# Optimization experiments

Hardware: AMD Instinct MI355X
Metric: run time of the kernel (lower is better)

## Reference

```python
import jax, jax.numpy as jnp
import numpy as np

HID = 128          # hidden_dim
NF = 8             # n_features of reconstructed PathFeatureExtractor
S0 = 100.0
T = 1.0
XI0 = 0.235 ** 2
ETA_REF = 1.9
DELTA_IDX = 3      # PathFeatureExtractor.DELTA_PREV_INDEX
NEG_SLOPE = 0.2


def _features(S):
    """Causal per-step path features. S: (B, n+1) -> (B, n, NF)."""
    B, np1 = S.shape
    n = np1 - 1
    logm = jnp.log(S / S0)                       # (B, n+1) log-moneyness
    x = logm[:, :n]                              # value at step k
    ret = jnp.diff(logm, axis=1)                 # (B, n) log returns
    qv_full = jnp.cumsum(ret ** 2, axis=1)
    qv = jnp.concatenate([jnp.zeros((B, 1), S.dtype), qv_full[:, :-1]], axis=1)  # QV up to step k
    k = jnp.arange(n, dtype=S.dtype)
    t = k / n * T
    tau = (T - t) / T                            # normalized time to maturity
    run_mean = jnp.cumsum(x, axis=1) / (k + 1.0)
    ones = jnp.ones_like(x)
    feats = jnp.stack([
        x,                                       # 0: log(S_k/S0)
        tau * ones,                              # 1: time to maturity
        jnp.sqrt(XI0) * ones,                    # 2: ref vol
        jnp.zeros_like(x),                       # 3: delta_prev slot (injected in scan)
        run_mean,                                # 4: running mean log-price (sig level 1)
        qv,                                      # 5: realized quadratic variation (sig level 2 diag)
        ETA_REF * jnp.sqrt(qv + 1e-12),          # 6: vol-of-vol scaled QV
        (t / T) * ones,                          # 7: elapsed time
    ], axis=-1)
    return feats


def _mlp(feat, W0, b0, rW1, rb1, rW2, rb2, sW1, sb1, sW2, sb2, Wf, bf):
    lrelu = lambda v: jax.nn.leaky_relu(v, NEG_SLOPE)
    h = lrelu(feat @ W0 + b0)
    h = h + (lrelu(h @ rW1 + rb1) @ rW2 + rb2)   # ResidualBlock 1
    h = h + (lrelu(h @ sW1 + sb1) @ sW2 + sb2)   # ResidualBlock 2
    return jax.nn.sigmoid(h @ Wf + bf)[:, 0]


def _linear_params(key, fan_in, fan_out):
    kw, kb = jax.random.split(key)
    bound = 1.0 / np.sqrt(fan_in)
    W = jax.random.uniform(kw, (fan_in, fan_out), jnp.float32, -bound, bound)
    b = jax.random.uniform(kb, (fan_out,), jnp.float32, -bound, bound)
    return W, b


def setup_inputs() -> dict:
    key = jax.random.key(0)
    ks = jax.random.split(key, 6)
    B, n = 32768, 64
    # GBM-like price paths starting at S0
    incr = 0.02 * jax.random.normal(ks[0], (B, n), jnp.float32)
    logpath = jnp.concatenate([jnp.zeros((B, 1), jnp.float32), jnp.cumsum(incr, axis=1)], axis=1)
    S = S0 * jnp.exp(logpath)
    W0, b0 = _linear_params(ks[1], NF, HID)
    rW1, rb1 = _linear_params(ks[2], HID, HID)
    rW2, rb2 = _linear_params(jax.random.fold_in(ks[2], 1), HID, HID)
    sW1, sb1 = _linear_params(ks[3], HID, HID)
    sW2, sb2 = _linear_params(jax.random.fold_in(ks[3], 1), HID, HID)
    Wf, bf = _linear_params(ks[4], HID, 1)
    return {"S": S, "W0": W0, "b0": b0, "rW1": rW1, "rb1": rb1, "rW2": rW2, "rb2": rb2,
            "sW1": sW1, "sb1": sb1, "sW2": sW2, "sb2": sb2, "Wf": Wf, "bf": bf}


def reference(S, W0, b0, rW1, rb1, rW2, rb2, sW1, sb1, sW2, sb2, Wf, bf):
    feats = _features(S).astype(jnp.float32)          # (B, n, NF)
    fT = jnp.transpose(feats, (1, 0, 2))              # (n, B, NF) for scan
    B = S.shape[0]

    def step(delta_prev, feat_k):
        # inject detached delta_{k-1} at feature index 3 (matches .detach())
        feat_k = feat_k.at[:, DELTA_IDX].set(jax.lax.stop_gradient(delta_prev))
        d = _mlp(feat_k, W0, b0, rW1, rb1, rW2, rb2, sW1, sb1, sW2, sb2, Wf, bf)
        return d, d

    _, deltas = jax.lax.scan(step, jnp.zeros((B,), jnp.float32), fT)
    return jnp.transpose(deltas)                      # (B, n)
```

## Files before the change

kernel.cpp:

```cpp
#include <hip/hip_runtime.h>
#include <math.h>

#define HID 128
#define NSTEPS 64
#define SLEN 65
#define THREADS 256
#define ROWS 64
#define ASTRIDE 136
#define FSTRIDE 40
#define DSTR 68

typedef _Float16 half8 __attribute__((ext_vector_type(8)));
typedef __fp16 fp16x2 __attribute__((ext_vector_type(2)));
typedef float floatx4 __attribute__((ext_vector_type(4)));

__global__ __launch_bounds__(THREADS, 2)
void hedger(const float* __restrict__ S,
            const float* __restrict__ W0,  const float* __restrict__ b0,
            const float* __restrict__ rW1, const float* __restrict__ rb1,
            const float* __restrict__ rW2, const float* __restrict__ rb2,
            const float* __restrict__ sW1, const float* __restrict__ sb1,
            const float* __restrict__ sW2, const float* __restrict__ sb2,
            const float* __restrict__ Wf,  const float* __restrict__ bfp,
            float* __restrict__ out)
{
  __shared__ __align__(16) _Float16 bufA[ROWS * ASTRIDE];
  __shared__ __align__(16) _Float16 bufB[ROWS * ASTRIDE];
  __shared__ __align__(16) _Float16 featb[ROWS * FSTRIDE];
  __shared__ __align__(16) _Float16 WfS[HID];
  __shared__ __align__(16) _Float16 Ws2S[HID];
  __shared__             float    CvalS;
  __shared__ __align__(16) float    Slds[ROWS * SLEN];
  __shared__ __align__(16) float    deltab[ROWS * DSTR];

  const int tid  = threadIdx.x;
  const int wave = tid >> 6;
  const int lane = tid & 63;
  const int l15  = lane & 15;
  const int quad = lane >> 4;
  const int n_base = wave * 32;
  const int r0 = blockIdx.x * ROWS;
  const int col0 = n_base + 2 * l15;

  half8 wfrag[3][4][2];
  {
    const float* Wm[3] = {rW1, rW2, sW1};
#pragma unroll
    for (int m = 0; m < 3; ++m)
#pragma unroll
      for (int kq = 0; kq < 4; ++kq)
#pragma unroll
        for (int nt = 0; nt < 2; ++nt) {
          const int n  = col0 + nt;
          const int kb = kq * 32 + quad * 8;
          half8 f;
#pragma unroll
          for (int j = 0; j < 8; ++j)
            f[j] = (_Float16)Wm[m][(kb + j) * HID + n];
          wfrag[m][kq][nt] = f;
        }
  }
  half8 w0frag[2];
#pragma unroll
  for (int nt = 0; nt < 2; ++nt) {
    const int n = col0 + nt;
    half8 f;
#pragma unroll
    for (int j = 0; j < 8; ++j) {
      const int k = quad * 8 + j;
      f[j] = (k < 8) ? (_Float16)W0[k * HID + n] : (_Float16)0.f;
    }
    w0frag[nt] = f;
  }
  float b0r[2], rb1r[2], rb2r[2], sb1r[2];
#pragma unroll
  for (int nt = 0; nt < 2; ++nt) {
    const int n = col0 + nt;
    b0r[nt] = b0[n]; rb1r[nt] = rb1[n]; rb2r[nt] = rb2[n]; sb1r[nt] = sb1[n];
  }

  for (int i = tid; i < ROWS * FSTRIDE; i += THREADS) featb[i] = (_Float16)0.f;
  if (tid < HID) {
    WfS[tid] = (_Float16)Wf[tid];
    float s = 0.f;
    for (int n = 0; n < HID; ++n) s += sW2[tid * HID + n] * Wf[n];
    Ws2S[tid] = (_Float16)s;
  }
  if (wave == 0) {
    float p = sb2[lane] * Wf[lane] + sb2[lane + 64] * Wf[lane + 64];
    p += __shfl_xor(p, 1);  p += __shfl_xor(p, 2);  p += __shfl_xor(p, 4);
    p += __shfl_xor(p, 8);  p += __shfl_xor(p, 16); p += __shfl_xor(p, 32);
    if (lane == 0) CvalS = p + bfp[0];
  }
  for (int i = tid; i < ROWS * SLEN; i += THREADS)
    Slds[i] = S[(size_t)r0 * SLEN + i];
  __syncthreads();
  const float Cval = CvalS;

  float lm_prev = 0.f, cum_x = 0.f, qv = 0.f;
  const float* Srow = &Slds[(tid & (ROWS - 1)) * SLEN];
  if (tid < ROWS) {
    const float lm = logf(Srow[0] * 0.01f);
    lm_prev = lm; cum_x = lm; qv = 0.f;
    _Float16* fr = &featb[tid * FSTRIDE];
    fr[0] = (_Float16)lm;
    fr[1] = (_Float16)1.0f;
    fr[2] = (_Float16)0.235f;
    fr[3] = (_Float16)0.f;
    fr[4] = (_Float16)lm;
    fr[5] = (_Float16)0.f;
    fr[6] = (_Float16)(1.9f * sqrtf(1e-12f));
    fr[7] = (_Float16)0.f;
  }
  __syncthreads();

  floatx4 acc[4][2];

#define INIT_BIAS(BR) do { \
  _Pragma("unroll") for (int mt = 0; mt < 4; ++mt) \
  _Pragma("unroll") for (int nt = 0; nt < 2; ++nt) { \
    floatx4 z = {BR[nt], BR[nt], BR[nt], BR[nt]}; acc[mt][nt] = z; } } while (0)

#define INIT_BIAS_RES(BR, RESBUF) do { \
  _Pragma("unroll") for (int mt = 0; mt < 4; ++mt) \
  _Pragma("unroll") for (int r = 0; r < 4; ++r) { \
    const int row = mt * 16 + quad * 4 + r; \
    const fp16x2 h2 = *(const fp16x2*)&RESBUF[row * ASTRIDE + col0]; \
    acc[mt][0][r] = BR[0] + (float)h2[0]; \
    acc[mt][1][r] = BR[1] + (float)h2[1]; \
  } } while (0)

#define GEMM128(SRC, MI) do { \
  _Pragma("unroll") for (int kq = 0; kq < 4; ++kq) { \
    half8 afr[4]; \
    _Pragma("unroll") for (int mt = 0; mt < 4; ++mt) \
      afr[mt] = *(const half8*)&SRC[(mt * 16 + l15) * ASTRIDE + kq * 32 + quad * 8]; \
    _Pragma("unroll") for (int mt = 0; mt < 4; ++mt) \
    _Pragma("unroll") for (int nt = 0; nt < 2; ++nt) \
      acc[mt][nt] = __builtin_amdgcn_mfma_f32_16x16x32_f16( \
          afr[mt], wfrag[MI][kq][nt], acc[mt][nt], 0, 0, 0); \
  } } while (0)

#define EPI_LRELU(DST) do { \
  _Pragma("unroll") for (int mt = 0; mt < 4; ++mt) \
  _Pragma("unroll") for (int r = 0; r < 4; ++r) { \
    const int row = mt * 16 + quad * 4 + r; \
    const float v0 = acc[mt][0][r]; \
    const float v1 = acc[mt][1][r]; \
    fp16x2 h2 = {(__fp16)fmaxf(v0, 0.2f * v0), (__fp16)fmaxf(v1, 0.2f * v1)}; \
    *(fp16x2*)&DST[row * ASTRIDE + col0] = h2; \
  } } while (0)

#define EPI_STORE(DST) do { \
  _Pragma("unroll") for (int mt = 0; mt < 4; ++mt) \
  _Pragma("unroll") for (int r = 0; r < 4; ++r) { \
    const int row = mt * 16 + quad * 4 + r; \
    fp16x2 h2 = {(__fp16)acc[mt][0][r], (__fp16)acc[mt][1][r]}; \
    *(fp16x2*)&DST[row * ASTRIDE + col0] = h2; \
  } } while (0)

#pragma unroll 1
  for (int k = 0; k < NSTEPS; ++k) {
    INIT_BIAS(b0r);
    {
      half8 afr[4];
#pragma unroll
      for (int mt = 0; mt < 4; ++mt)
        afr[mt] = *(const half8*)&featb[(mt * 16 + l15) * FSTRIDE + quad * 8];
#pragma unroll
      for (int mt = 0; mt < 4; ++mt)
#pragma unroll
        for (int nt = 0; nt < 2; ++nt)
          acc[mt][nt] = __builtin_amdgcn_mfma_f32_16x16x32_f16(
              afr[mt], w0frag[nt], acc[mt][nt], 0, 0, 0);
    }
    EPI_LRELU(bufA);
    __syncthreads();

    if (tid < ROWS) {
      const int kk = k + 1;
      const float lm = logf(Srow[kk] * 0.01f);
      const float rr = lm - lm_prev; qv += rr * rr;
      lm_prev = lm; cum_x += lm;
      const float tT = (float)kk * (1.f / 64.f);
      _Float16* fr = &featb[tid * FSTRIDE];
      fr[0] = (_Float16)lm;
      fr[1] = (_Float16)(1.f - tT);
      fr[4] = (_Float16)(cum_x / (float)(kk + 1));
      fr[5] = (_Float16)qv;
      fr[6] = (_Float16)(1.9f * sqrtf(qv + 1e-12f));
      fr[7] = (_Float16)tT;
    }

    INIT_BIAS(rb1r);            GEMM128(bufA, 0); EPI_LRELU(bufB);
    __syncthreads();
    INIT_BIAS_RES(rb2r, bufA);  GEMM128(bufB, 1); EPI_STORE(bufA);
    __syncthreads();
    INIT_BIAS(sb1r);            GEMM128(bufA, 2); EPI_LRELU(bufB);
    __syncthreads();

    {
      floatx4 dacc  = {0.f, 0.f, 0.f, 0.f};
      floatx4 dacc2 = {0.f, 0.f, 0.f, 0.f};
#pragma unroll
      for (int kq = 0; kq < 4; ++kq) {
        const int off = kq * 32 + quad * 8;
        const half8 a1 = *(const half8*)&bufA[(wave * 16 + l15) * ASTRIDE + off];
        const half8 w1 = *(const half8*)&WfS[off];
        dacc  = __builtin_amdgcn_mfma_f32_16x16x32_f16(a1, w1, dacc, 0, 0, 0);
        const half8 a2 = *(const half8*)&bufB[(wave * 16 + l15) * ASTRIDE + off];
        const half8 w2 = *(const half8*)&Ws2S[off];
        dacc2 = __builtin_amdgcn_mfma_f32_16x16x32_f16(a2, w2, dacc2, 0, 0, 0);
      }
      if (l15 < 4) {
        const float s1 = (l15 & 2) ? ((l15 & 1) ? dacc[3] : dacc[2])
                                   : ((l15 & 1) ? dacc[1] : dacc[0]);
        const float s2 = (l15 & 2) ? ((l15 & 1) ? dacc2[3] : dacc2[2])
                                   : ((l15 & 1) ? dacc2[1] : dacc2[0]);
        const int row = wave * 16 + quad * 4 + l15;
        const float d = 1.f / (1.f + expf(-(s1 + s2 + Cval)));
        featb[row * FSTRIDE + 3] = (_Float16)d;
        deltab[row * DSTR + k] = d;
      }
    }
    __syncthreads();
  }

  {
    const int row = tid >> 2;
    const int c0  = (tid & 3) * 16;
    const float* dr = &deltab[row * DSTR + c0];
    float* orow = &out[(size_t)(r0 + row) * NSTEPS + c0];
#pragma unroll
    for (int u = 0; u < 4; ++u) {
      const floatx4 v = *(const floatx4*)&dr[u * 4];
      *(floatx4*)&orow[u * 4] = v;
    }
  }
#undef INIT_BIAS
#undef INIT_BIAS_RES
#undef GEMM128
#undef EPI_LRELU
#undef EPI_STORE
}

extern "C" void kernel_launch(void* const* d_in, const int* in_sizes, int n_in,
                              void* d_out, int out_size, void* d_ws, size_t ws_size,
                              hipStream_t stream) {
  const float* S   = (const float*)d_in[0];
  const float* W0  = (const float*)d_in[1];
  const float* b0  = (const float*)d_in[2];
  const float* rW1 = (const float*)d_in[3];
  const float* rb1 = (const float*)d_in[4];
  const float* rW2 = (const float*)d_in[5];
  const float* rb2 = (const float*)d_in[6];
  const float* sW1 = (const float*)d_in[7];
  const float* sb1 = (const float*)d_in[8];
  const float* sW2 = (const float*)d_in[9];
  const float* sb2 = (const float*)d_in[10];
  const float* Wf  = (const float*)d_in[11];
  const float* bf  = (const float*)d_in[12];
  float* out = (float*)d_out;

  const int B = out_size / NSTEPS;
  const int nblocks = B / ROWS;
  hedger<<<nblocks, THREADS, 0, stream>>>(
      S, W0, b0, rW1, rb1, rW2, rb2, sW1, sb1, sW2, sb2, Wf, bf, out);
}
```

Baseline: 345.6 us.

## Fold residual block's second linear into next layer weights to drop a barrier

Precomputes rW2·sW1 per block as a fused weight, so the second residual block's pre-activation becomes bufA·sW1 + bufB·(rW2·sW1) + (rb2·sW1 + sb1). The per-step stage that materialised h after block 1 is removed, along with one barrier per step. The final readout adds a third dot product using rW2·Wf, plus the matching bias constant. It also drops the S staging in LDS and reads S directly from global memory. The trade-off is more LDS (a third buffer), an extra fp16 rounding of the fused weights, and a per-block setup GEMM.

```diff
diff --git a/kernel.cpp b/kernel.cpp
--- a/kernel.cpp
+++ b/kernel.cpp
@@ -26,11 +26,12 @@
 {
   __shared__ __align__(16) _Float16 bufA[ROWS * ASTRIDE];
   __shared__ __align__(16) _Float16 bufB[ROWS * ASTRIDE];
+  __shared__ __align__(16) _Float16 bufC[ROWS * ASTRIDE];
   __shared__ __align__(16) _Float16 featb[ROWS * FSTRIDE];
   __shared__ __align__(16) _Float16 WfS[HID];
+  __shared__ __align__(16) _Float16 WfuS[HID];
   __shared__ __align__(16) _Float16 Ws2S[HID];
   __shared__             float    CvalS;
-  __shared__ __align__(16) float    Slds[ROWS * SLEN];
   __shared__ __align__(16) float    deltab[ROWS * DSTR];
 
   const int tid  = threadIdx.x;
@@ -44,9 +45,9 @@
 
   half8 wfrag[3][4][2];
   {
-    const float* Wm[3] = {rW1, rW2, sW1};
-#pragma unroll
-    for (int m = 0; m < 3; ++m)
+    const float* Wm[2] = {rW1, sW1};
+#pragma unroll
+    for (int m = 0; m < 2; ++m)
 #pragma unroll
       for (int kq = 0; kq < 4; ++kq)
 #pragma unroll
@@ -72,33 +73,113 @@
     }
     w0frag[nt] = f;
   }
-  float b0r[2], rb1r[2], rb2r[2], sb1r[2];
+  float b0r[2], rb1r[2], cv[2];
 #pragma unroll
   for (int nt = 0; nt < 2; ++nt) {
     const int n = col0 + nt;
-    b0r[nt] = b0[n]; rb1r[nt] = rb1[n]; rb2r[nt] = rb2[n]; sb1r[nt] = sb1[n];
+    b0r[nt] = b0[n]; rb1r[nt] = rb1[n];
+    float p = 0.f;
+#pragma unroll
+    for (int kq = 0; kq < 4; ++kq) {
+      const int kb = kq * 32 + quad * 8;
+#pragma unroll
+      for (int j = 0; j < 8; ++j)
+        p += rb2[kb + j] * (float)wfrag[1][kq][nt][j];
+    }
+    p += __shfl_xor(p, 16);
+    p += __shfl_xor(p, 32);
+    cv[nt] = p + sb1[n];
   }
 
   for (int i = tid; i < ROWS * FSTRIDE; i += THREADS) featb[i] = (_Float16)0.f;
   if (tid < HID) {
     WfS[tid] = (_Float16)Wf[tid];
-    float s = 0.f;
-    for (int n = 0; n < HID; ++n) s += sW2[tid * HID + n] * Wf[n];
-    Ws2S[tid] = (_Float16)s;
+    float su = 0.f, ss = 0.f;
+    for (int n = 0; n < HID; ++n) {
+      su += rW2[tid * HID + n] * Wf[n];
+      ss += sW2[tid * HID + n] * Wf[n];
+    }
+    WfuS[tid] = (_Float16)su;
+    Ws2S[tid] = (_Float16)ss;
   }
   if (wave == 0) {
-    float p = sb2[lane] * Wf[lane] + sb2[lane + 64] * Wf[lane + 64];
+    float p = (rb2[lane] + sb2[lane]) * Wf[lane]
+            + (rb2[lane + 64] + sb2[lane + 64]) * Wf[lane + 64];
     p += __shfl_xor(p, 1);  p += __shfl_xor(p, 2);  p += __shfl_xor(p, 4);
     p += __shfl_xor(p, 8);  p += __shfl_xor(p, 16); p += __shfl_xor(p, 32);
     if (lane == 0) CvalS = p + bfp[0];
   }
-  for (int i = tid; i < ROWS * SLEN; i += THREADS)
-    Slds[i] = S[(size_t)r0 * SLEN + i];
+
+  floatx4 acc[4][2];
+
+#define INIT_BIAS(BR) do { \
+  _Pragma("unroll") for (int mt = 0; mt < 4; ++mt) \
+  _Pragma("unroll") for (int nt = 0; nt < 2; ++nt) { \
+    floatx4 z = {BR[nt], BR[nt], BR[nt], BR[nt]}; acc[mt][nt] = z; } } while (0)
+
+#define GEMM128(SRC, MI) do { \
+  _Pragma("unroll") for (int kq = 0; kq < 4; ++kq) { \
+    half8 afr[4]; \
+    _Pragma("unroll") for (int mt = 0; mt < 4; ++mt) \
+      afr[mt] = *(const half8*)&SRC[(mt * 16 + l15) * ASTRIDE + kq * 32 + quad * 8]; \
+    _Pragma("unroll") for (int mt = 0; mt < 4; ++mt) \
+    _Pragma("unroll") for (int nt = 0; nt < 2; ++nt) \
+      acc[mt][nt] = __builtin_amdgcn_mfma_f32_16x16x32_f16( \
+          afr[mt], wfrag[MI][kq][nt], acc[mt][nt], 0, 0, 0); \
+  } } while (0)
+
+#define EPI_LRELU(DST) do { \
+  _Pragma("unroll") for (int mt = 0; mt < 4; ++mt) \
+  _Pragma("unroll") for (int r = 0; r < 4; ++r) { \
+    const int row = mt * 16 + quad * 4 + r; \
+    const float v0 = acc[mt][0][r]; \
+    const float v1 = acc[mt][1][r]; \
+    fp16x2 h2 = {(__fp16)fmaxf(v0, 0.2f * v0), (__fp16)fmaxf(v1, 0.2f * v1)}; \
+    *(fp16x2*)&DST[row * ASTRIDE + col0] = h2; \
+  } } while (0)
+
+#define EPI_STORE(DST) do { \
+  _Pragma("unroll") for (int mt = 0; mt < 4; ++mt) \
+  _Pragma("unroll") for (int r = 0; r < 4; ++r) { \
+    const int row = mt * 16 + quad * 4 + r; \
+    fp16x2 h2 = {(__fp16)acc[mt][0][r], (__fp16)acc[mt][1][r]}; \
+    *(fp16x2*)&DST[row * ASTRIDE + col0] = h2; \
+  } } while (0)
+
+#pragma unroll 1
+  for (int h = 0; h < 2; ++h) {
+    __syncthreads();
+    for (int i = tid; i < ROWS * HID; i += THREADS) {
+      const int row = i >> 7, c = i & 127;
+      bufA[row * ASTRIDE + c] = (_Float16)rW2[(h * 64 + row) * HID + c];
+    }
+    __syncthreads();
+    {
+      float zr[2] = {0.f, 0.f};
+      INIT_BIAS(zr);
+      GEMM128(bufA, 1);
+      EPI_STORE(bufB);
+    }
+    __syncthreads();
+#pragma unroll
+    for (int kqh = 0; kqh < 2; ++kqh) {
+      const int kq = h * 2 + kqh;
+      half8 f0, f1;
+#pragma unroll
+      for (int j = 0; j < 8; ++j) {
+        const int kl = kq * 32 + quad * 8 + j - h * 64;
+        const fp16x2 p = *(const fp16x2*)&bufB[kl * ASTRIDE + col0];
+        f0[j] = (_Float16)p[0];
+        f1[j] = (_Float16)p[1];
+      }
+      wfrag[2][kq][0] = f0;
+      wfrag[2][kq][1] = f1;
+    }
+  }
   __syncthreads();
-  const float Cval = CvalS;
 
   float lm_prev = 0.f, cum_x = 0.f, qv = 0.f;
-  const float* Srow = &Slds[(tid & (ROWS - 1)) * SLEN];
+  const float* Srow = S + (size_t)(r0 + (tid & (ROWS - 1))) * SLEN;
   if (tid < ROWS) {
     const float lm = logf(Srow[0] * 0.01f);
     lm_prev = lm; cum_x = lm; qv = 0.f;
@@ -113,51 +194,7 @@
     fr[7] = (_Float16)0.f;
   }
   __syncthreads();
-
-  floatx4 acc[4][2];
-
-#define INIT_BIAS(BR) do { \
-  _Pragma("unroll") for (int mt = 0; mt < 4; ++mt) \
-  _Pragma("unroll") for (int nt = 0; nt < 2; ++nt) { \
-    floatx4 z = {BR[nt], BR[nt], BR[nt], BR[nt]}; acc[mt][nt] = z; } } while (0)
-
-#define INIT_BIAS_RES(BR, RESBUF) do { \
-  _Pragma("unroll") for (int mt = 0; mt < 4; ++mt) \
-  _Pragma("unroll") for (int r = 0; r < 4; ++r) { \
-    const int row = mt * 16 + quad * 4 + r; \
-    const fp16x2 h2 = *(const fp16x2*)&RESBUF[row * ASTRIDE + col0]; \
-    acc[mt][0][r] = BR[0] + (float)h2[0]; \
-    acc[mt][1][r] = BR[1] + (float)h2[1]; \
-  } } while (0)
-
-#define GEMM128(SRC, MI) do { \
-  _Pragma("unroll") for (int kq = 0; kq < 4; ++kq) { \
-    half8 afr[4]; \
-    _Pragma("unroll") for (int mt = 0; mt < 4; ++mt) \
-      afr[mt] = *(const half8*)&SRC[(mt * 16 + l15) * ASTRIDE + kq * 32 + quad * 8]; \
-    _Pragma("unroll") for (int mt = 0; mt < 4; ++mt) \
-    _Pragma("unroll") for (int nt = 0; nt < 2; ++nt) \
-      acc[mt][nt] = __builtin_amdgcn_mfma_f32_16x16x32_f16( \
-          afr[mt], wfrag[MI][kq][nt], acc[mt][nt], 0, 0, 0); \
-  } } while (0)
-
-#define EPI_LRELU(DST) do { \
-  _Pragma("unroll") for (int mt = 0; mt < 4; ++mt) \
-  _Pragma("unroll") for (int r = 0; r < 4; ++r) { \
-    const int row = mt * 16 + quad * 4 + r; \
-    const float v0 = acc[mt][0][r]; \
-    const float v1 = acc[mt][1][r]; \
-    fp16x2 h2 = {(__fp16)fmaxf(v0, 0.2f * v0), (__fp16)fmaxf(v1, 0.2f * v1)}; \
-    *(fp16x2*)&DST[row * ASTRIDE + col0] = h2; \
-  } } while (0)
-
-#define EPI_STORE(DST) do { \
-  _Pragma("unroll") for (int mt = 0; mt < 4; ++mt) \
-  _Pragma("unroll") for (int r = 0; r < 4; ++r) { \
-    const int row = mt * 16 + quad * 4 + r; \
-    fp16x2 h2 = {(__fp16)acc[mt][0][r], (__fp16)acc[mt][1][r]}; \
-    *(fp16x2*)&DST[row * ASTRIDE + col0] = h2; \
-  } } while (0)
+  const float Cval = CvalS;
 
 #pragma unroll 1
   for (int k = 0; k < NSTEPS; ++k) {
@@ -192,33 +229,42 @@
       fr[7] = (_Float16)tT;
     }
 
-    INIT_BIAS(rb1r);            GEMM128(bufA, 0); EPI_LRELU(bufB);
-    __syncthreads();
-    INIT_BIAS_RES(rb2r, bufA);  GEMM128(bufB, 1); EPI_STORE(bufA);
-    __syncthreads();
-    INIT_BIAS(sb1r);            GEMM128(bufA, 2); EPI_LRELU(bufB);
+    INIT_BIAS(rb1r);  GEMM128(bufA, 0);  EPI_LRELU(bufB);
+    __syncthreads();
+
+    INIT_BIAS(cv);
+    GEMM128(bufA, 1);
+    GEMM128(bufB, 2);
+    EPI_LRELU(bufC);
     __syncthreads();
 
     {
-      floatx4 dacc  = {0.f, 0.f, 0.f, 0.f};
-      floatx4 dacc2 = {0.f, 0.f, 0.f, 0.f};
+      floatx4 d1 = {0.f, 0.f, 0.f, 0.f};
+      floatx4 d2 = {0.f, 0.f, 0.f, 0.f};
+      floatx4 d3 = {0.f, 0.f, 0.f, 0.f};
+      const int arow = (wave * 16 + l15) * ASTRIDE;
 #pragma unroll
       for (int kq = 0; kq < 4; ++kq) {
         const int off = kq * 32 + quad * 8;
-        const half8 a1 = *(const half8*)&bufA[(wave * 16 + l15) * ASTRIDE + off];
+        const half8 a1 = *(const half8*)&bufA[arow + off];
         const half8 w1 = *(const half8*)&WfS[off];
-        dacc  = __builtin_amdgcn_mfma_f32_16x16x32_f16(a1, w1, dacc, 0, 0, 0);
-        const half8 a2 = *(const half8*)&bufB[(wave * 16 + l15) * ASTRIDE + off];
-        const half8 w2 = *(const half8*)&Ws2S[off];
-        dacc2 = __builtin_amdgcn_mfma_f32_16x16x32_f16(a2, w2, dacc2, 0, 0, 0);
+        d1 = __builtin_amdgcn_mfma_f32_16x16x32_f16(a1, w1, d1, 0, 0, 0);
+        const half8 a2 = *(const half8*)&bufB[arow + off];
+        const half8 w2 = *(const half8*)&WfuS[off];
+        d2 = __builtin_amdgcn_mfma_f32_16x16x32_f16(a2, w2, d2, 0, 0, 0);
+        const half8 a3 = *(const half8*)&bufC[arow + off];
+        const half8 w3 = *(const half8*)&Ws2S[off];
+        d3 = __builtin_amdgcn_mfma_f32_16x16x32_f16(a3, w3, d3, 0, 0, 0);
       }
       if (l15 < 4) {
-        const float s1 = (l15 & 2) ? ((l15 & 1) ? dacc[3] : dacc[2])
-                                   : ((l15 & 1) ? dacc[1] : dacc[0]);
-        const float s2 = (l15 & 2) ? ((l15 & 1) ? dacc2[3] : dacc2[2])
-                                   : ((l15 & 1) ? dacc2[1] : dacc2[0]);
+        const float s1 = (l15 & 2) ? ((l15 & 1) ? d1[3] : d1[2])
+                                   : ((l15 & 1) ? d1[1] : d1[0]);
+        const float s2 = (l15 & 2) ? ((l15 & 1) ? d2[3] : d2[2])
+                                   : ((l15 & 1) ? d2[1] : d2[0]);
+        const float s3 = (l15 & 2) ? ((l15 & 1) ? d3[3] : d3[2])
+                                   : ((l15 & 1) ? d3[1] : d3[0]);
         const int row = wave * 16 + quad * 4 + l15;
-        const float d = 1.f / (1.f + expf(-(s1 + s2 + Cval)));
+        const float d = 1.f / (1.f + expf(-(s1 + s2 + s3 + Cval)));
         featb[row * FSTRIDE + 3] = (_Float16)d;
         deltab[row * DSTR + k] = d;
       }
@@ -238,7 +284,6 @@
     }
   }
 #undef INIT_BIAS
-#undef INIT_BIAS_RES
 #undef GEMM128
 #undef EPI_LRELU
 #undef EPI_STORE
```

After: 588.4 us. 1.7x slower.
